# Performance work log

Hardware: AMD Instinct MI355X
Metric: run time of the kernel (lower is better)

Reference implementation:

```python
import jax, jax.numpy as jnp
import numpy as np

N = 4096
IN_F = 256
OUT_F = 64
HEADS = 4
EDGE_F = 32
ALPHA = 0.2  # leaky relu negative slope


def setup_inputs() -> dict:
    key = jax.random.key(0)
    k1, k2, k3, k4, k5 = jax.random.split(key, 5)
    h = jax.random.normal(k1, (N, IN_F), dtype=jnp.float32)
    adj = jax.random.randint(k2, (N, N, 1), 0, 2, dtype=jnp.int32)
    edge_attr = jax.random.normal(k3, (N, EDGE_F), dtype=jnp.float32)
    # xavier-uniform-ish params
    W = jax.random.normal(k4, (IN_F, HEADS * OUT_F), dtype=jnp.float32) * 0.1
    a = jax.random.normal(k5, (HEADS, 2 * OUT_F + EDGE_F, 1), dtype=jnp.float32) * 0.1
    return {"h": h, "adj": adj, "edge_attr": edge_attr, "W": W, "a": a}


def reference(h, adj, edge_attr, W, a):
    n = h.shape[0]
    Wh = (h @ W).reshape(n, HEADS, OUT_F)            # [N, H, O]
    a_vec = a[:, :, 0]                               # [H, 2O+E]
    a_src = a_vec[:, :OUT_F]                         # [H, O]
    a_dst = a_vec[:, OUT_F:2 * OUT_F]                # [H, O]
    a_edge = a_vec[:, 2 * OUT_F:]                    # [H, E]
    # decompose the all-pairs concat dot-product: score(i,j,h) =
    #   a_src.Wh[i] + a_dst.Wh[j] + a_edge.edge_attr[j]  (edge term follows repeat(N,1) semantics)
    src = jnp.einsum('nho,ho->nh', Wh, a_src)        # [N, H]
    dst = jnp.einsum('nho,ho->nh', Wh, a_dst)        # [N, H]
    edg = jnp.einsum('ne,he->nh', edge_attr, a_edge) # [N, H]
    e = jax.nn.leaky_relu(src[:, None, :] + (dst + edg)[None, :, :],
                          negative_slope=ALPHA)       # [N, N, H]
    att = jnp.where(adj > 0, e, jnp.zeros((), e.dtype))
    att = jax.nn.softmax(att, axis=1)                # softmax over neighbors j
    # dropout p=0.0 (eval): no-op
    h_prime = jnp.einsum('ijh,jho->iho', att, Wh)    # [N, H, O]
    return jax.nn.elu(h_prime.reshape(n, HEADS * OUT_F))
```

## Files before the change

kernel.cpp:

```cpp
#include <hip/hip_runtime.h>
#include <hip/hip_bf16.h>
#include <math.h>

#define NN 4096
#define IN_F 256
#define OUT_F 64
#define HEADS 4
#define EDGE_F 32
#define HO 256
#define AVEC 160
#define ALPHA 0.2f
#define LOG2E 1.44269504088896f

typedef __attribute__((ext_vector_type(8))) short bf16x8;
typedef __attribute__((ext_vector_type(4))) float f32x4;

__device__ __forceinline__ float exp2fast(float x) {
    return __builtin_amdgcn_exp2f(x);
}

__device__ __forceinline__ unsigned short f2bf(float x) {
    unsigned u = __float_as_uint(x);
    u += 0x7FFF + ((u >> 16) & 1);
    return (unsigned short)(u >> 16);
}

__global__ __launch_bounds__(256) void k_pack(const int* __restrict__ adj,
                                              unsigned* __restrict__ abitsT) {
    __shared__ unsigned bits[32][16];
    const int tid = threadIdx.x;
    const int w = tid >> 6, l = tid & 63;
    const int ib = blockIdx.x >> 2, js = blockIdx.x & 3;
    const int i0 = ib * 16;
    const int jbase = js * 1024 + w * 256;
    const int* base = adj + (size_t)i0 * NN + jbase + l;

#pragma unroll
    for (int half = 0; half < 2; ++half) {
        int vv[32];
#pragma unroll
        for (int t = 0; t < 32; ++t) {
            const int ii = (t & 7) + half * 8;
            const int r = t >> 3;
            vv[t] = base[(size_t)ii * NN + r * 64];
        }
#pragma unroll
        for (int t = 0; t < 32; ++t) {
            const int ii = (t & 7) + half * 8;
            const int r = t >> 3;
            const unsigned long long m = __ballot(vv[t] > 0);
            const int jwl = w * 8 + r * 2;
            if (l == 0) bits[jwl][ii] = (unsigned)m;
            else if (l == 1) bits[jwl + 1][ii] = (unsigned)(m >> 32);
        }
    }
    __syncthreads();
#pragma unroll
    for (int t = tid; t < 32 * 16; t += 256) {
        const int jwl = t >> 4, ii = t & 15;
        abitsT[(size_t)(js * 32 + jwl) * NN + i0 + ii] = bits[jwl][ii];
    }
}

__global__ __launch_bounds__(256) void k_wh(const float* __restrict__ h,
                                            const float* __restrict__ W,
                                            const float* __restrict__ a,
                                            const float* __restrict__ edge_attr,
                                            unsigned short* __restrict__ pk,
                                            float* __restrict__ src,
                                            float* __restrict__ cdpT) {
    __shared__ float hs[32][32];
    __shared__ float Ws[32][64];
    const int tid = threadIdx.x;
    const int jb = blockIdx.x >> 2, hd = blockIdx.x & 3;
    const int n0 = jb * 32;
    const int rg = tid >> 6, cl = tid & 63;
    float acc[8];
#pragma unroll
    for (int r = 0; r < 8; ++r) acc[r] = 0.f;

    for (int kc = 0; kc < IN_F; kc += 32) {
        {
            const int r = tid >> 3, k4 = (tid & 7) << 2;
            *(float4*)&hs[r][k4] = *(const float4*)&h[(size_t)(n0 + r) * IN_F + kc + k4];
        }
#pragma unroll
        for (int q = 0; q < 2; ++q) {
            const int f = tid + q * 256;
            const int k = f >> 4, c4 = (f & 15) << 2;
            *(float4*)&Ws[k][c4] = *(const float4*)&W[(size_t)(kc + k) * HO + hd * 64 + c4];
        }
        __syncthreads();
#pragma unroll
        for (int k = 0; k < 32; ++k) {
            const float wv = Ws[k][cl];
#pragma unroll
            for (int r = 0; r < 8; ++r)
                acc[r] = fmaf(hs[rg * 8 + r][k], wv, acc[r]);
        }
        __syncthreads();
    }

    {
        const int g = cl >> 4, lr = cl & 15;
        unsigned short* fb = pk + ((size_t)(jb * HEADS + hd) * 4 + g) * 512;
        bf16x8 v;
#pragma unroll
        for (int r = 0; r < 8; ++r) v[r] = (short)f2bf(acc[r]);
        *(bf16x8*)(fb + (rg * 16 + lr) * 8) = v;
    }

    const float asrc = a[hd * AVEC + cl];
    const float adst = a[hd * AVEC + OUT_F + cl];
    float s_keep = 0.f, d_keep = 0.f;
#pragma unroll
    for (int r = 0; r < 8; ++r) {
        float sp = acc[r] * asrc;
        float dp = acc[r] * adst;
#pragma unroll
        for (int off = 32; off >= 1; off >>= 1) {
            sp += __shfl_xor(sp, off);
            dp += __shfl_xor(dp, off);
        }
        if (cl == r) { s_keep = sp; d_keep = dp; }
    }
    if (cl < 8) {
        const int i = n0 + rg * 8 + cl;
        float eg = 0.f;
        const float* erow = edge_attr + (size_t)i * EDGE_F;
#pragma unroll
        for (int e4 = 0; e4 < EDGE_F; e4 += 4) {
            const float4 ev = *(const float4*)(erow + e4);
            const float4 av = *(const float4*)(a + hd * AVEC + 2 * OUT_F + e4);
            eg = fmaf(ev.x, av.x, fmaf(ev.y, av.y, fmaf(ev.z, av.z, fmaf(ev.w, av.w, eg))));
        }
        src[i * HEADS + hd] = s_keep * LOG2E;
        cdpT[(size_t)hd * NN + i] = (d_keep + eg) * LOG2E;
    }
}

__global__ __launch_bounds__(512, 8) void k_pv(const unsigned* __restrict__ abitsT,
                                               const unsigned short* __restrict__ pk,
                                               const float* __restrict__ src,
                                               const float* __restrict__ cdpT,
                                               float* __restrict__ out) {
    __shared__ float plds[8][16][65];
    __shared__ float lsum[8][16];
    const int tid = threadIdx.x;
    const int js = tid >> 6, l = tid & 63;
    const int ib = blockIdx.x >> 2, hd = blockIdx.x & 3;
    const int i0 = ib * 16;
    const int lr = l & 15, kb = l >> 4;
    const int i = i0 + lr;
    const float si = src[i * HEADS + hd];
    const float* crow = cdpT + (size_t)hd * NN + kb * 8;
    const unsigned short* pkb = pk + (size_t)hd * 2048 + l * 8;

    bf16x8 bones;
#pragma unroll
    for (int r = 0; r < 8; ++r) bones[r] = (short)0x3F80;

    f32x4 acc0 = {0.f, 0.f, 0.f, 0.f};
    f32x4 acc1 = {0.f, 0.f, 0.f, 0.f};
    f32x4 acc2 = {0.f, 0.f, 0.f, 0.f};
    f32x4 acc3 = {0.f, 0.f, 0.f, 0.f};
    f32x4 accL = {0.f, 0.f, 0.f, 0.f};

    for (int jt = js * 32; jt < NN; jt += 256) {
        const unsigned wbits = abitsT[(size_t)(jt >> 5) * NN + i];
        const unsigned byte = (wbits >> (kb * 8)) & 0xFFu;
        const float4 c0 = *(const float4*)(crow + jt);
        const float4 c1 = *(const float4*)(crow + jt + 4);
        const unsigned short* fb = pkb + (size_t)(jt >> 5) * (HEADS * 4 * 512);
        const bf16x8 b0 = *(const bf16x8*)(fb);
        const bf16x8 b1 = *(const bf16x8*)(fb + 512);
        const bf16x8 b2 = *(const bf16x8*)(fb + 1024);
        const bf16x8 b3 = *(const bf16x8*)(fb + 1536);
        float e, p0, p1, p2, p3, p4, p5, p6, p7;
        e = si + c0.x; e = fmaxf(e, ALPHA * e); e = (byte &   1u) ? e : 0.f; p0 = exp2fast(e);
        e = si + c0.y; e = fmaxf(e, ALPHA * e); e = (byte &   2u) ? e : 0.f; p1 = exp2fast(e);
        e = si + c0.z; e = fmaxf(e, ALPHA * e); e = (byte &   4u) ? e : 0.f; p2 = exp2fast(e);
        e = si + c0.w; e = fmaxf(e, ALPHA * e); e = (byte &   8u) ? e : 0.f; p3 = exp2fast(e);
        e = si + c1.x; e = fmaxf(e, ALPHA * e); e = (byte &  16u) ? e : 0.f; p4 = exp2fast(e);
        e = si + c1.y; e = fmaxf(e, ALPHA * e); e = (byte &  32u) ? e : 0.f; p5 = exp2fast(e);
        e = si + c1.z; e = fmaxf(e, ALPHA * e); e = (byte &  64u) ? e : 0.f; p6 = exp2fast(e);
        e = si + c1.w; e = fmaxf(e, ALPHA * e); e = (byte & 128u) ? e : 0.f; p7 = exp2fast(e);
        bf16x8 af;
        af[0] = (short)f2bf(p0); af[1] = (short)f2bf(p1);
        af[2] = (short)f2bf(p2); af[3] = (short)f2bf(p3);
        af[4] = (short)f2bf(p4); af[5] = (short)f2bf(p5);
        af[6] = (short)f2bf(p6); af[7] = (short)f2bf(p7);
        acc0 = __builtin_amdgcn_mfma_f32_16x16x32_bf16(af, b0, acc0, 0, 0, 0);
        acc1 = __builtin_amdgcn_mfma_f32_16x16x32_bf16(af, b1, acc1, 0, 0, 0);
        acc2 = __builtin_amdgcn_mfma_f32_16x16x32_bf16(af, b2, acc2, 0, 0, 0);
        acc3 = __builtin_amdgcn_mfma_f32_16x16x32_bf16(af, b3, acc3, 0, 0, 0);
        accL = __builtin_amdgcn_mfma_f32_16x16x32_bf16(af, bones, accL, 0, 0, 0);
    }

    if (lr == 0) {
#pragma unroll
        for (int r = 0; r < 4; ++r)
            lsum[js][kb * 4 + r] = accL[r];
    }
#pragma unroll
    for (int r = 0; r < 4; ++r) {
        const int row = kb * 4 + r;
        plds[js][row][ 0 + lr] = acc0[r];
        plds[js][row][16 + lr] = acc1[r];
        plds[js][row][32 + lr] = acc2[r];
        plds[js][row][48 + lr] = acc3[r];
    }
    __syncthreads();

    const int row = tid >> 5, cp = (tid & 31) * 2;
    float L = 0.f, x0 = 0.f, x1 = 0.f;
#pragma unroll
    for (int p = 0; p < 8; ++p) {
        L  += lsum[p][row];
        x0 += plds[p][row][cp];
        x1 += plds[p][row][cp + 1];
    }
    const float inv = 1.f / L;
    float2 o;
    float x;
    x = x0 * inv; o.x = x > 0.f ? x : (__expf(x) - 1.f);
    x = x1 * inv; o.y = x > 0.f ? x : (__expf(x) - 1.f);
    *(float2*)(out + (size_t)(i0 + row) * HO + hd * 64 + cp) = o;
}

extern "C" void kernel_launch(void* const* d_in, const int* in_sizes, int n_in,
                              void* d_out, int out_size, void* d_ws, size_t ws_size,
                              hipStream_t stream) {
    const float* h         = (const float*)d_in[0];
    const int*   adj       = (const int*)d_in[1];
    const float* edge_attr = (const float*)d_in[2];
    const float* W         = (const float*)d_in[3];
    const float* a         = (const float*)d_in[4];
    float* out = (float*)d_out;

    unsigned short* pk     = (unsigned short*)d_ws;
    float*          cdpT   = (float*)(pk + (size_t)NN * HO);
    float*          src    = cdpT + (size_t)HEADS * NN;
    unsigned*       abitsT = (unsigned*)(src + (size_t)NN * HEADS);

    k_pack<<<256 * 4, 256, 0, stream>>>(adj, abitsT);
    k_wh<<<128 * HEADS, 256, 0, stream>>>(h, W, a, edge_attr, pk, src, cdpT);
    k_pv<<<256 * 4, 512, 0, stream>>>(abitsT, pk, src, cdpT, out);
}
```

Before: 157.6 us.

## Merge adjacency packing and Wh projection into one launch; use native bf16 conversion

The adjacency bit-packing kernel and the Wh/score projection kernel become a single launch, with block ranges dispatched by blockIdx and shared memory held in a union. This removes one kernel launch and lets the two independent prep stages run on the GPU at the same time. Separately, the manual float-to-bf16 rounding in the attention inner loop is replaced by native __bf16 casts, which may map to hardware conversion instructions. The merged kernel's register and LDS footprint is the larger of the two branches, which could lower occupancy for the packing blocks.

```diff
diff --git a/kernel.cpp b/kernel.cpp
--- a/kernel.cpp
+++ b/kernel.cpp
@@ -13,6 +13,7 @@
 #define LOG2E 1.44269504088896f
 
 typedef __attribute__((ext_vector_type(8))) short bf16x8;
+typedef __attribute__((ext_vector_type(8))) __bf16 bfv8;
 typedef __attribute__((ext_vector_type(4))) float f32x4;
 
 __device__ __forceinline__ float exp2fast(float x) {
@@ -25,54 +26,55 @@
     return (unsigned short)(u >> 16);
 }
 
-__global__ __launch_bounds__(256) void k_pack(const int* __restrict__ adj,
+__global__ __launch_bounds__(256) void k_prep(const float* __restrict__ h,
+                                              const float* __restrict__ W,
+                                              const float* __restrict__ a,
+                                              const float* __restrict__ edge_attr,
+                                              const int* __restrict__ adj,
+                                              unsigned short* __restrict__ pk,
+                                              float* __restrict__ src,
+                                              float* __restrict__ cdpT,
                                               unsigned* __restrict__ abitsT) {
-    __shared__ unsigned bits[32][16];
+    __shared__ union {
+        unsigned bits[32][16];
+        struct { float hs[32][32]; float Ws[32][64]; } gw;
+    } sm;
     const int tid = threadIdx.x;
-    const int w = tid >> 6, l = tid & 63;
-    const int ib = blockIdx.x >> 2, js = blockIdx.x & 3;
-    const int i0 = ib * 16;
-    const int jbase = js * 1024 + w * 256;
-    const int* base = adj + (size_t)i0 * NN + jbase + l;
-
-#pragma unroll
-    for (int half = 0; half < 2; ++half) {
-        int vv[32];
-#pragma unroll
-        for (int t = 0; t < 32; ++t) {
-            const int ii = (t & 7) + half * 8;
-            const int r = t >> 3;
-            vv[t] = base[(size_t)ii * NN + r * 64];
-        }
-#pragma unroll
-        for (int t = 0; t < 32; ++t) {
-            const int ii = (t & 7) + half * 8;
-            const int r = t >> 3;
-            const unsigned long long m = __ballot(vv[t] > 0);
-            const int jwl = w * 8 + r * 2;
-            if (l == 0) bits[jwl][ii] = (unsigned)m;
-            else if (l == 1) bits[jwl + 1][ii] = (unsigned)(m >> 32);
-        }
-    }
-    __syncthreads();
-#pragma unroll
-    for (int t = tid; t < 32 * 16; t += 256) {
-        const int jwl = t >> 4, ii = t & 15;
-        abitsT[(size_t)(js * 32 + jwl) * NN + i0 + ii] = bits[jwl][ii];
-    }
-}
-
-__global__ __launch_bounds__(256) void k_wh(const float* __restrict__ h,
-                                            const float* __restrict__ W,
-                                            const float* __restrict__ a,
-                                            const float* __restrict__ edge_attr,
-                                            unsigned short* __restrict__ pk,
-                                            float* __restrict__ src,
-                                            float* __restrict__ cdpT) {
-    __shared__ float hs[32][32];
-    __shared__ float Ws[32][64];
-    const int tid = threadIdx.x;
-    const int jb = blockIdx.x >> 2, hd = blockIdx.x & 3;
+    if (blockIdx.x < 1024) {
+        const int w = tid >> 6, l = tid & 63;
+        const int ib = blockIdx.x >> 2, js = blockIdx.x & 3;
+        const int i0 = ib * 16;
+        const int jbase = js * 1024 + w * 256;
+        const int* base = adj + (size_t)i0 * NN + jbase + l;
+#pragma unroll
+        for (int half = 0; half < 2; ++half) {
+            int vv[32];
+#pragma unroll
+            for (int t = 0; t < 32; ++t) {
+                const int ii = (t & 7) + half * 8;
+                const int r = t >> 3;
+                vv[t] = base[(size_t)ii * NN + r * 64];
+            }
+#pragma unroll
+            for (int t = 0; t < 32; ++t) {
+                const int ii = (t & 7) + half * 8;
+                const int r = t >> 3;
+                const unsigned long long m = __ballot(vv[t] > 0);
+                const int jwl = w * 8 + r * 2;
+                if (l == 0) sm.bits[jwl][ii] = (unsigned)m;
+                else if (l == 1) sm.bits[jwl + 1][ii] = (unsigned)(m >> 32);
+            }
+        }
+        __syncthreads();
+#pragma unroll
+        for (int t = tid; t < 32 * 16; t += 256) {
+            const int jwl = t >> 4, ii = t & 15;
+            abitsT[(size_t)(js * 32 + jwl) * NN + i0 + ii] = sm.bits[jwl][ii];
+        }
+        return;
+    }
+    const int b = blockIdx.x - 1024;
+    const int jb = b >> 2, hd = b & 3;
     const int n0 = jb * 32;
     const int rg = tid >> 6, cl = tid & 63;
     float acc[8];
@@ -82,21 +84,21 @@
     for (int kc = 0; kc < IN_F; kc += 32) {
         {
             const int r = tid >> 3, k4 = (tid & 7) << 2;
-            *(float4*)&hs[r][k4] = *(const float4*)&h[(size_t)(n0 + r) * IN_F + kc + k4];
+            *(float4*)&sm.gw.hs[r][k4] = *(const float4*)&h[(size_t)(n0 + r) * IN_F + kc + k4];
         }
 #pragma unroll
         for (int q = 0; q < 2; ++q) {
             const int f = tid + q * 256;
             const int k = f >> 4, c4 = (f & 15) << 2;
-            *(float4*)&Ws[k][c4] = *(const float4*)&W[(size_t)(kc + k) * HO + hd * 64 + c4];
+            *(float4*)&sm.gw.Ws[k][c4] = *(const float4*)&W[(size_t)(kc + k) * HO + hd * 64 + c4];
         }
         __syncthreads();
 #pragma unroll
         for (int k = 0; k < 32; ++k) {
-            const float wv = Ws[k][cl];
+            const float wv = sm.gw.Ws[k][cl];
 #pragma unroll
             for (int r = 0; r < 8; ++r)
-                acc[r] = fmaf(hs[rg * 8 + r][k], wv, acc[r]);
+                acc[r] = fmaf(sm.gw.hs[rg * 8 + r][k], wv, acc[r]);
         }
         __syncthreads();
     }
@@ -185,11 +187,12 @@
         e = si + c1.y; e = fmaxf(e, ALPHA * e); e = (byte &  32u) ? e : 0.f; p5 = exp2fast(e);
         e = si + c1.z; e = fmaxf(e, ALPHA * e); e = (byte &  64u) ? e : 0.f; p6 = exp2fast(e);
         e = si + c1.w; e = fmaxf(e, ALPHA * e); e = (byte & 128u) ? e : 0.f; p7 = exp2fast(e);
-        bf16x8 af;
-        af[0] = (short)f2bf(p0); af[1] = (short)f2bf(p1);
-        af[2] = (short)f2bf(p2); af[3] = (short)f2bf(p3);
-        af[4] = (short)f2bf(p4); af[5] = (short)f2bf(p5);
-        af[6] = (short)f2bf(p6); af[7] = (short)f2bf(p7);
+        bfv8 afb;
+        afb[0] = (__bf16)p0; afb[1] = (__bf16)p1;
+        afb[2] = (__bf16)p2; afb[3] = (__bf16)p3;
+        afb[4] = (__bf16)p4; afb[5] = (__bf16)p5;
+        afb[6] = (__bf16)p6; afb[7] = (__bf16)p7;
+        const bf16x8 af = __builtin_bit_cast(bf16x8, afb);
         acc0 = __builtin_amdgcn_mfma_f32_16x16x32_bf16(af, b0, acc0, 0, 0, 0);
         acc1 = __builtin_amdgcn_mfma_f32_16x16x32_bf16(af, b1, acc1, 0, 0, 0);
         acc2 = __builtin_amdgcn_mfma_f32_16x16x32_bf16(af, b2, acc2, 0, 0, 0);
@@ -243,7 +246,6 @@
     float*          src    = cdpT + (size_t)HEADS * NN;
     unsigned*       abitsT = (unsigned*)(src + (size_t)NN * HEADS);
 
-    k_pack<<<256 * 4, 256, 0, stream>>>(adj, abitsT);
-    k_wh<<<128 * HEADS, 256, 0, stream>>>(h, W, a, edge_attr, pk, src, cdpT);
+    k_prep<<<1024 + 512, 256, 0, stream>>>(h, W, a, edge_attr, adj, pk, src, cdpT, abitsT);
     k_pv<<<256 * 4, 512, 0, stream>>>(abitsT, pk, src, cdpT, out);
 }
```

New measurement: 170.1 us. 1.08x slower.
